# Kernel optimization log

Hardware: AMD Instinct MI355X
Metric: run time of the kernel (lower is better)

The kernel has to match this reference:

```python
import jax, jax.numpy as jnp
import numpy as np

NUM_GROUP = 512
GROUP_SIZE = 32


def setup_inputs() -> dict:
    key = jax.random.key(0)
    pts = jax.random.normal(key, (8, 8192, 6), dtype=jnp.float32)
    return {"pts": pts}


def _fps(xyz, num_group):
    """Farthest point sampling. xyz: (B, N, 3) -> indices (B, G)."""
    B, N, _ = xyz.shape

    def body(carry, _):
        dist, far = carry  # dist: (B, N) running min sq-dist to chosen set; far: (B,)
        centroid = jnp.take_along_axis(xyz, far[:, None, None], axis=1)  # (B, 1, 3)
        d = jnp.sum((xyz - centroid) ** 2, axis=-1)  # (B, N)
        dist = jnp.minimum(dist, d)
        new_far = jnp.argmax(dist, axis=-1)  # (B,)
        return (dist, new_far), far

    init = (jnp.full((B, N), 1e10, dtype=xyz.dtype), jnp.zeros((B,), dtype=jnp.int32))
    _, idxs = jax.lax.scan(body, init, None, length=num_group)  # (G, B)
    return idxs.T  # (B, G)


def _knn(k, xyz, center):
    """k nearest neighbors of each center among xyz. Returns idx (B, G, k)."""
    # squared distances (B, G, N)
    d2 = (jnp.sum(center ** 2, -1)[:, :, None]
          + jnp.sum(xyz ** 2, -1)[:, None, :]
          - 2.0 * jnp.einsum('bgc,bnc->bgn', center, xyz))
    _, idx = jax.lax.top_k(-d2, k)
    return idx


def reference(pts):
    xyz = pts[:, :, :3].astype(jnp.float32)
    fps_idx = _fps(xyz, NUM_GROUP)  # (B, G)
    center = jnp.take_along_axis(xyz, fps_idx[:, :, None], axis=1)  # (B, G, 3)
    idx = _knn(GROUP_SIZE, xyz, center)  # (B, G, K)
    # gather neighborhoods per batch: pts (B, N, C), idx (B, G, K) -> (B, G, K, C)
    neighborhood = jax.vmap(lambda p, i: p[i])(pts, idx)
    # center only the xyz channels
    nb_xyz = neighborhood[..., :3] - center[:, :, None, :]
    neighborhood = jnp.concatenate([nb_xyz, neighborhood[..., 3:]], axis=-1)
    return (neighborhood, center)
```

## Files before the change

### kernel.cpp

```cpp
#include <hip/hip_runtime.h>
#include <stdint.h>

#define BATCH 8
#define NPTS 8192
#define NGRP 512
#define KNN 32
#define NCH 6

#define FPS_T 512
#define FPS_PPT (NPTS / FPS_T)
#define PAIRS (FPS_PPT / 2)
#define FPS_NW (FPS_T / 64)

typedef float f2 __attribute__((ext_vector_type(2)));

__device__ __forceinline__ f2 pk_add(f2 a, f2 b) {
    f2 d;
    asm("v_pk_add_f32 %0, %1, %2" : "=v"(d) : "v"(a), "v"(b));
    return d;
}
__device__ __forceinline__ f2 pk_mul(f2 a, f2 b) {
    f2 d;
    asm("v_pk_mul_f32 %0, %1, %2" : "=v"(d) : "v"(a), "v"(b));
    return d;
}

template <int CTRL>
__device__ __forceinline__ float dpp_fmax(float v) {
    int s = __builtin_amdgcn_update_dpp(__float_as_int(v), __float_as_int(v),
                                        CTRL, 0xF, 0xF, false);
    return fmaxf(v, __int_as_float(s));
}

__global__ __launch_bounds__(FPS_T) void fps_kernel(const float* __restrict__ pts,
                                                    float* __restrict__ out_ctr) {
    __shared__ float xs[NPTS], ys[NPTS], zs[NPTS];
    __shared__ float ctr_lds[NGRP * 3];
    __shared__ float wslot[FPS_NW];
    __shared__ unsigned int islot[2];

    const int b   = blockIdx.x;
    const int tid = threadIdx.x;
    const float* base = pts + (size_t)b * NPTS * NCH;

    f2 x2[PAIRS], y2[PAIRS], z2[PAIRS], dist2[PAIRS];
#pragma unroll
    for (int i = 0; i < PAIRS; ++i) {
        int p0 = tid + (2 * i) * FPS_T;
        int p1 = tid + (2 * i + 1) * FPS_T;
        float xa = base[p0 * NCH + 0], ya = base[p0 * NCH + 1], za = base[p0 * NCH + 2];
        float xb = base[p1 * NCH + 0], yb = base[p1 * NCH + 1], zb = base[p1 * NCH + 2];
        x2[i] = (f2){xa, xb};
        y2[i] = (f2){ya, yb};
        z2[i] = (f2){za, zb};
        dist2[i] = (f2){1e10f, 1e10f};
        xs[p0] = xa; ys[p0] = ya; zs[p0] = za;
        xs[p1] = xb; ys[p1] = yb; zs[p1] = zb;
    }
    __syncthreads();

    int far = 0;
    const int wid  = tid >> 6;
    const int lane = tid & 63;

    for (int g = 0; g < NGRP; ++g) {
        float cx = xs[far], cy = ys[far], cz = zs[far];
        if (tid == 0) {
            ctr_lds[g * 3 + 0] = cx;
            ctr_lds[g * 3 + 1] = cy;
            ctr_lds[g * 3 + 2] = cz;
            islot[g & 1] = 0xFFFFFFFFu;
        }
        f2 ncx = (f2){-cx, -cx};
        f2 ncy = (f2){-cy, -cy};
        f2 ncz = (f2){-cz, -cz};

        float bestv = -1.0f;
#pragma unroll
        for (int i = 0; i < PAIRS; ++i) {
            f2 dx = pk_add(x2[i], ncx);
            f2 dy = pk_add(y2[i], ncy);
            f2 dz = pk_add(z2[i], ncz);
            f2 sx = pk_mul(dx, dx);
            f2 sy = pk_mul(dy, dy);
            f2 t  = pk_add(sx, sy);
            f2 sz = pk_mul(dz, dz);
            f2 d  = pk_add(t, sz);
            float nd0 = fminf(dist2[i].x, d.x);
            float nd1 = fminf(dist2[i].y, d.y);
            dist2[i].x = nd0;
            dist2[i].y = nd1;
            bestv = fmaxf(fmaxf(nd0, nd1), bestv);
        }

        float m = bestv;
        m = dpp_fmax<0x111>(m);
        m = dpp_fmax<0x112>(m);
        m = dpp_fmax<0x114>(m);
        m = dpp_fmax<0x118>(m);
        m = dpp_fmax<0x142>(m);
        m = dpp_fmax<0x143>(m);
        if (lane == 63) wslot[wid] = m;
        __syncthreads();

        float M = wslot[0];
#pragma unroll
        for (int w = 1; w < FPS_NW; ++w) M = fmaxf(M, wslot[w]);

        if (bestv == M) {
            int bj = 0;
#pragma unroll
            for (int i = PAIRS - 1; i >= 0; --i) {
                if (dist2[i].y == M) bj = 2 * i + 1;
                if (dist2[i].x == M) bj = 2 * i;
            }
            atomicMin(&islot[g & 1], (unsigned)(tid + bj * FPS_T));
        }
        __syncthreads();
        far = (int)islot[g & 1];
    }

    float* ctr = out_ctr + (size_t)b * NGRP * 3;
    for (int i = tid; i < NGRP * 3; i += FPS_T) ctr[i] = ctr_lds[i];
}

__device__ __forceinline__ unsigned long long knn_key(const float* __restrict__ base,
                                                      int p, float cx, float cy,
                                                      float cz, float cc) {
    float x = base[p * NCH + 0];
    float y = base[p * NCH + 1];
    float z = base[p * NCH + 2];
    float xx = __fadd_rn(__fadd_rn(__fmul_rn(x, x), __fmul_rn(y, y)), __fmul_rn(z, z));
    float dt = fmaf(cz, z, fmaf(cy, y, __fmul_rn(cx, x)));
    float d2 = __fsub_rn(__fadd_rn(cc, xx), __fmul_rn(2.0f, dt));
    unsigned int bits = __float_as_uint(d2);
    unsigned int ord = bits ^ ((unsigned)((int)bits >> 31) | 0x80000000u);
    return ((unsigned long long)ord << 13) | (unsigned)p;
}

__global__ __launch_bounds__(64) void knn_kernel(const float* __restrict__ pts,
                                                 const float* __restrict__ ctr,
                                                 float* __restrict__ out_nb) {
    const int bg   = blockIdx.x;
    const int b    = bg >> 9;
    const int lane = threadIdx.x & 63;
    const float* base = pts + (size_t)b * NPTS * NCH;

    const float cx = ctr[bg * 3 + 0];
    const float cy = ctr[bg * 3 + 1];
    const float cz = ctr[bg * 3 + 2];
    const float cc = __fadd_rn(__fadd_rn(__fmul_rn(cx, cx), __fmul_rn(cy, cy)),
                               __fmul_rn(cz, cz));

    unsigned long long R = knn_key(base, lane, cx, cy, cz, cc);
#pragma unroll
    for (int k = 2; k <= 64; k <<= 1) {
#pragma unroll
        for (int j = k >> 1; j > 0; j >>= 1) {
            unsigned long long o = __shfl_xor(R, j, 64);
            bool takeMin = (((lane & k) == 0) == ((lane & j) == 0));
            unsigned long long mn = (o < R) ? o : R;
            unsigned long long mx = (o < R) ? R : o;
            R = takeMin ? mn : mx;
        }
    }
    unsigned long long R31 = __shfl(R, 31, 64);

    for (int c = 1; c < NPTS / 64; ++c) {
        unsigned long long key = knn_key(base, c * 64 + lane, cx, cy, cz, cc);
        unsigned long long qual = __ballot(key < R31);
        while (qual) {
            int src = __ffsll(qual) - 1;
            qual &= qual - 1;
            unsigned long long bk = __shfl(key, src, 64);
            int rank = __popcll(__ballot(R < bk));
            unsigned long long Rp = __shfl_up(R, 1, 64);
            R = (lane == rank) ? bk : ((lane > rank) ? Rp : R);
            R31 = __shfl(R, 31, 64);
        }
    }

    if (lane < KNN) {
        int idx = (int)(R & 8191ULL);
        const float* s = base + (size_t)idx * NCH;
        float* d = out_nb + ((size_t)bg * KNN + lane) * NCH;
        d[0] = s[0] - cx;
        d[1] = s[1] - cy;
        d[2] = s[2] - cz;
        d[3] = s[3];
        d[4] = s[4];
        d[5] = s[5];
    }
}

extern "C" void kernel_launch(void* const* d_in, const int* in_sizes, int n_in,
                              void* d_out, int out_size, void* d_ws, size_t ws_size,
                              hipStream_t stream) {
    const float* pts = (const float*)d_in[0];
    float* out = (float*)d_out;
    float* out_nb  = out;
    float* out_ctr = out + (size_t)BATCH * NGRP * KNN * NCH;

    hipLaunchKernelGGL(fps_kernel, dim3(BATCH), dim3(FPS_T), 0, stream, pts, out_ctr);
    hipLaunchKernelGGL(knn_kernel, dim3(BATCH * NGRP), dim3(64), 0, stream,
                       pts, out_ctr, out_nb);
}
```

Baseline: 572.7 us.

## Fuse FPS and KNN into persistent kernel overlapping via global flags

Merges the farthest-point-sampling and KNN kernels into one persistent launch. Eight blocks run FPS and publish each chosen index to a workspace flag array, while the remaining blocks' waves spin on those flags and start KNN for each center as soon as it is available, overlapping the serial FPS with KNN work. FPS block size drops to 256 threads, and the argmax now reduces a packed 64-bit value/index key with DPP, removing the second barrier and the LDS atomicMin. This depends on all blocks being co-resident to avoid deadlock, and it adds a memset plus polling overhead.

```diff
diff --git a/kernel.cpp b/kernel.cpp
--- a/kernel.cpp
+++ b/kernel.cpp
@@ -7,10 +7,13 @@
 #define KNN 32
 #define NCH 6
 
-#define FPS_T 512
+#define FPS_T 256
 #define FPS_PPT (NPTS / FPS_T)
 #define PAIRS (FPS_PPT / 2)
 #define FPS_NW (FPS_T / 64)
+
+#define NBLK 248
+#define KNN_WAVES ((NBLK - BATCH) * FPS_NW)
 
 typedef float f2 __attribute__((ext_vector_type(2)));
 
@@ -26,102 +29,14 @@
 }
 
 template <int CTRL>
-__device__ __forceinline__ float dpp_fmax(float v) {
-    int s = __builtin_amdgcn_update_dpp(__float_as_int(v), __float_as_int(v),
-                                        CTRL, 0xF, 0xF, false);
-    return fmaxf(v, __int_as_float(s));
-}
-
-__global__ __launch_bounds__(FPS_T) void fps_kernel(const float* __restrict__ pts,
-                                                    float* __restrict__ out_ctr) {
-    __shared__ float xs[NPTS], ys[NPTS], zs[NPTS];
-    __shared__ float ctr_lds[NGRP * 3];
-    __shared__ float wslot[FPS_NW];
-    __shared__ unsigned int islot[2];
-
-    const int b   = blockIdx.x;
-    const int tid = threadIdx.x;
-    const float* base = pts + (size_t)b * NPTS * NCH;
-
-    f2 x2[PAIRS], y2[PAIRS], z2[PAIRS], dist2[PAIRS];
-#pragma unroll
-    for (int i = 0; i < PAIRS; ++i) {
-        int p0 = tid + (2 * i) * FPS_T;
-        int p1 = tid + (2 * i + 1) * FPS_T;
-        float xa = base[p0 * NCH + 0], ya = base[p0 * NCH + 1], za = base[p0 * NCH + 2];
-        float xb = base[p1 * NCH + 0], yb = base[p1 * NCH + 1], zb = base[p1 * NCH + 2];
-        x2[i] = (f2){xa, xb};
-        y2[i] = (f2){ya, yb};
-        z2[i] = (f2){za, zb};
-        dist2[i] = (f2){1e10f, 1e10f};
-        xs[p0] = xa; ys[p0] = ya; zs[p0] = za;
-        xs[p1] = xb; ys[p1] = yb; zs[p1] = zb;
-    }
-    __syncthreads();
-
-    int far = 0;
-    const int wid  = tid >> 6;
-    const int lane = tid & 63;
-
-    for (int g = 0; g < NGRP; ++g) {
-        float cx = xs[far], cy = ys[far], cz = zs[far];
-        if (tid == 0) {
-            ctr_lds[g * 3 + 0] = cx;
-            ctr_lds[g * 3 + 1] = cy;
-            ctr_lds[g * 3 + 2] = cz;
-            islot[g & 1] = 0xFFFFFFFFu;
-        }
-        f2 ncx = (f2){-cx, -cx};
-        f2 ncy = (f2){-cy, -cy};
-        f2 ncz = (f2){-cz, -cz};
-
-        float bestv = -1.0f;
-#pragma unroll
-        for (int i = 0; i < PAIRS; ++i) {
-            f2 dx = pk_add(x2[i], ncx);
-            f2 dy = pk_add(y2[i], ncy);
-            f2 dz = pk_add(z2[i], ncz);
-            f2 sx = pk_mul(dx, dx);
-            f2 sy = pk_mul(dy, dy);
-            f2 t  = pk_add(sx, sy);
-            f2 sz = pk_mul(dz, dz);
-            f2 d  = pk_add(t, sz);
-            float nd0 = fminf(dist2[i].x, d.x);
-            float nd1 = fminf(dist2[i].y, d.y);
-            dist2[i].x = nd0;
-            dist2[i].y = nd1;
-            bestv = fmaxf(fmaxf(nd0, nd1), bestv);
-        }
-
-        float m = bestv;
-        m = dpp_fmax<0x111>(m);
-        m = dpp_fmax<0x112>(m);
-        m = dpp_fmax<0x114>(m);
-        m = dpp_fmax<0x118>(m);
-        m = dpp_fmax<0x142>(m);
-        m = dpp_fmax<0x143>(m);
-        if (lane == 63) wslot[wid] = m;
-        __syncthreads();
-
-        float M = wslot[0];
-#pragma unroll
-        for (int w = 1; w < FPS_NW; ++w) M = fmaxf(M, wslot[w]);
-
-        if (bestv == M) {
-            int bj = 0;
-#pragma unroll
-            for (int i = PAIRS - 1; i >= 0; --i) {
-                if (dist2[i].y == M) bj = 2 * i + 1;
-                if (dist2[i].x == M) bj = 2 * i;
-            }
-            atomicMin(&islot[g & 1], (unsigned)(tid + bj * FPS_T));
-        }
-        __syncthreads();
-        far = (int)islot[g & 1];
-    }
-
-    float* ctr = out_ctr + (size_t)b * NGRP * 3;
-    for (int i = tid; i < NGRP * 3; i += FPS_T) ctr[i] = ctr_lds[i];
+__device__ __forceinline__ unsigned long long dpp_max64(unsigned long long k) {
+    int lo = (int)(unsigned)k;
+    int hi = (int)(unsigned)(k >> 32);
+    int plo = __builtin_amdgcn_update_dpp(lo, lo, CTRL, 0xF, 0xF, false);
+    int phi = __builtin_amdgcn_update_dpp(hi, hi, CTRL, 0xF, 0xF, false);
+    unsigned long long o =
+        ((unsigned long long)(unsigned)phi << 32) | (unsigned)plo;
+    return (o > k) ? o : k;
 }
 
 __device__ __forceinline__ unsigned long long knn_key(const float* __restrict__ base,
@@ -138,58 +53,168 @@
     return ((unsigned long long)ord << 13) | (unsigned)p;
 }
 
-__global__ __launch_bounds__(64) void knn_kernel(const float* __restrict__ pts,
-                                                 const float* __restrict__ ctr,
-                                                 float* __restrict__ out_nb) {
-    const int bg   = blockIdx.x;
-    const int b    = bg >> 9;
-    const int lane = threadIdx.x & 63;
-    const float* base = pts + (size_t)b * NPTS * NCH;
-
-    const float cx = ctr[bg * 3 + 0];
-    const float cy = ctr[bg * 3 + 1];
-    const float cz = ctr[bg * 3 + 2];
-    const float cc = __fadd_rn(__fadd_rn(__fmul_rn(cx, cx), __fmul_rn(cy, cy)),
-                               __fmul_rn(cz, cz));
-
-    unsigned long long R = knn_key(base, lane, cx, cy, cz, cc);
-#pragma unroll
-    for (int k = 2; k <= 64; k <<= 1) {
-#pragma unroll
-        for (int j = k >> 1; j > 0; j >>= 1) {
-            unsigned long long o = __shfl_xor(R, j, 64);
-            bool takeMin = (((lane & k) == 0) == ((lane & j) == 0));
-            unsigned long long mn = (o < R) ? o : R;
-            unsigned long long mx = (o < R) ? R : o;
-            R = takeMin ? mn : mx;
+__global__ __launch_bounds__(FPS_T) void fused_kernel(const float* __restrict__ pts,
+                                                      float* __restrict__ out_ctr,
+                                                      float* __restrict__ out_nb,
+                                                      unsigned int* __restrict__ faridx,
+                                                      int fstride) {
+    __shared__ float xs[NPTS], ys[NPTS], zs[NPTS];
+    __shared__ float ctr_lds[NGRP * 3];
+    __shared__ unsigned long long slots[2][FPS_NW];
+
+    const int tid = threadIdx.x;
+
+    if (blockIdx.x < BATCH) {
+        const int b = blockIdx.x;
+        const float* base = pts + (size_t)b * NPTS * NCH;
+
+        f2 x2[PAIRS], y2[PAIRS], z2[PAIRS], dist2[PAIRS];
+#pragma unroll
+        for (int i = 0; i < PAIRS; ++i) {
+            int p0 = tid + (2 * i) * FPS_T;
+            int p1 = tid + (2 * i + 1) * FPS_T;
+            float xa = base[p0 * NCH + 0], ya = base[p0 * NCH + 1], za = base[p0 * NCH + 2];
+            float xb = base[p1 * NCH + 0], yb = base[p1 * NCH + 1], zb = base[p1 * NCH + 2];
+            x2[i] = (f2){xa, xb};
+            y2[i] = (f2){ya, yb};
+            z2[i] = (f2){za, zb};
+            dist2[i] = (f2){1e10f, 1e10f};
+            xs[p0] = xa; ys[p0] = ya; zs[p0] = za;
+            xs[p1] = xb; ys[p1] = yb; zs[p1] = zb;
         }
-    }
-    unsigned long long R31 = __shfl(R, 31, 64);
-
-    for (int c = 1; c < NPTS / 64; ++c) {
-        unsigned long long key = knn_key(base, c * 64 + lane, cx, cy, cz, cc);
-        unsigned long long qual = __ballot(key < R31);
-        while (qual) {
-            int src = __ffsll(qual) - 1;
-            qual &= qual - 1;
-            unsigned long long bk = __shfl(key, src, 64);
-            int rank = __popcll(__ballot(R < bk));
-            unsigned long long Rp = __shfl_up(R, 1, 64);
-            R = (lane == rank) ? bk : ((lane > rank) ? Rp : R);
-            R31 = __shfl(R, 31, 64);
+        __syncthreads();
+
+        int far = 0;
+        const int wid  = tid >> 6;
+        const int lane = tid & 63;
+
+        for (int g = 0; g < NGRP; ++g) {
+            float cx = xs[far], cy = ys[far], cz = zs[far];
+            if (tid == 0) {
+                ctr_lds[g * 3 + 0] = cx;
+                ctr_lds[g * 3 + 1] = cy;
+                ctr_lds[g * 3 + 2] = cz;
+                __hip_atomic_store(&faridx[(b * NGRP + g) * fstride], (unsigned)far,
+                                   __ATOMIC_RELAXED, __HIP_MEMORY_SCOPE_AGENT);
+            }
+            if (g == NGRP - 1) break;
+
+            f2 ncx = (f2){-cx, -cx};
+            f2 ncy = (f2){-cy, -cy};
+            f2 ncz = (f2){-cz, -cz};
+
+            float bestv = -1.0f;
+            int bestj = 0;
+#pragma unroll
+            for (int i = 0; i < PAIRS; ++i) {
+                f2 dx = pk_add(x2[i], ncx);
+                f2 dy = pk_add(y2[i], ncy);
+                f2 dz = pk_add(z2[i], ncz);
+                f2 sx = pk_mul(dx, dx);
+                f2 sy = pk_mul(dy, dy);
+                f2 t  = pk_add(sx, sy);
+                f2 sz = pk_mul(dz, dz);
+                f2 d  = pk_add(t, sz);
+                float nd0 = fminf(dist2[i].x, d.x);
+                float nd1 = fminf(dist2[i].y, d.y);
+                dist2[i].x = nd0;
+                dist2[i].y = nd1;
+                if (nd0 > bestv) { bestv = nd0; bestj = 2 * i; }
+                if (nd1 > bestv) { bestv = nd1; bestj = 2 * i + 1; }
+            }
+            int bestp = tid + bestj * FPS_T;
+            unsigned long long key =
+                ((unsigned long long)__float_as_uint(bestv) << 13) |
+                (unsigned)(8191 - bestp);
+
+            key = dpp_max64<0x111>(key);
+            key = dpp_max64<0x112>(key);
+            key = dpp_max64<0x114>(key);
+            key = dpp_max64<0x118>(key);
+            key = dpp_max64<0x142>(key);
+            key = dpp_max64<0x143>(key);
+            if (lane == 63) slots[g & 1][wid] = key;
+            __syncthreads();
+
+            unsigned long long best = slots[g & 1][0];
+#pragma unroll
+            for (int w = 1; w < FPS_NW; ++w) {
+                unsigned long long o = slots[g & 1][w];
+                best = (o > best) ? o : best;
+            }
+            far = 8191 - (int)(best & 8191ULL);
         }
-    }
-
-    if (lane < KNN) {
-        int idx = (int)(R & 8191ULL);
-        const float* s = base + (size_t)idx * NCH;
-        float* d = out_nb + ((size_t)bg * KNN + lane) * NCH;
-        d[0] = s[0] - cx;
-        d[1] = s[1] - cy;
-        d[2] = s[2] - cz;
-        d[3] = s[3];
-        d[4] = s[4];
-        d[5] = s[5];
+
+        __syncthreads();
+        float* ctr = out_ctr + (size_t)b * NGRP * 3;
+        for (int i = tid; i < NGRP * 3; i += FPS_T) ctr[i] = ctr_lds[i];
+
+    } else {
+        const int wid  = tid >> 6;
+        const int lane = tid & 63;
+        const int W = (blockIdx.x - BATCH) * FPS_NW + wid;
+
+        for (int e = W; e < BATCH * NGRP; e += KNN_WAVES) {
+            const int g  = e >> 3;
+            const int b  = e & 7;
+            const int bg = b * NGRP + g;
+            const float* base = pts + (size_t)b * NPTS * NCH;
+
+            unsigned fidx;
+            if (lane == 0) {
+                while ((fidx = __hip_atomic_load(&faridx[bg * fstride],
+                                                 __ATOMIC_RELAXED,
+                                                 __HIP_MEMORY_SCOPE_AGENT)) == 0xFFFFFFFFu)
+                    __builtin_amdgcn_s_sleep(8);
+            }
+            fidx = (unsigned)__shfl((int)fidx, 0, 64);
+
+            const float cx = base[fidx * NCH + 0];
+            const float cy = base[fidx * NCH + 1];
+            const float cz = base[fidx * NCH + 2];
+            const float cc = __fadd_rn(__fadd_rn(__fmul_rn(cx, cx), __fmul_rn(cy, cy)),
+                                       __fmul_rn(cz, cz));
+
+            unsigned long long R = knn_key(base, lane, cx, cy, cz, cc);
+#pragma unroll
+            for (int k = 2; k <= 64; k <<= 1) {
+#pragma unroll
+                for (int j = k >> 1; j > 0; j >>= 1) {
+                    unsigned long long o = __shfl_xor(R, j, 64);
+                    bool takeMin = (((lane & k) == 0) == ((lane & j) == 0));
+                    unsigned long long mn = (o < R) ? o : R;
+                    unsigned long long mx = (o < R) ? R : o;
+                    R = takeMin ? mn : mx;
+                }
+            }
+            unsigned long long R31 = __shfl(R, 31, 64);
+
+            for (int c = 1; c < NPTS / 64; ++c) {
+                unsigned long long key = knn_key(base, c * 64 + lane, cx, cy, cz, cc);
+                unsigned long long qual = __ballot(key < R31);
+                while (qual) {
+                    int src = __ffsll(qual) - 1;
+                    qual &= qual - 1;
+                    unsigned long long bk = __shfl(key, src, 64);
+                    int rank = __popcll(__ballot(R < bk));
+                    unsigned long long Rp = __shfl_up(R, 1, 64);
+                    R = (lane == rank) ? bk : ((lane > rank) ? Rp : R);
+                    R31 = __shfl(R, 31, 64);
+                }
+            }
+
+            if (lane < KNN) {
+                int idx = (int)(R & 8191ULL);
+                const float* s = base + (size_t)idx * NCH;
+                float* d = out_nb + ((size_t)bg * KNN + lane) * NCH;
+                d[0] = s[0] - cx;
+                d[1] = s[1] - cy;
+                d[2] = s[2] - cz;
+                d[3] = s[3];
+                d[4] = s[4];
+                d[5] = s[5];
+            }
+        }
     }
 }
 
@@ -201,7 +226,11 @@
     float* out_nb  = out;
     float* out_ctr = out + (size_t)BATCH * NGRP * KNN * NCH;
 
-    hipLaunchKernelGGL(fps_kernel, dim3(BATCH), dim3(FPS_T), 0, stream, pts, out_ctr);
-    hipLaunchKernelGGL(knn_kernel, dim3(BATCH * NGRP), dim3(64), 0, stream,
-                       pts, out_ctr, out_nb);
-}
+    const size_t nctr = (size_t)BATCH * NGRP;
+    int fstride = (ws_size >= nctr * 16 * sizeof(unsigned)) ? 16 : 1;
+    unsigned int* faridx = (unsigned int*)d_ws;
+
+    hipMemsetAsync(d_ws, 0xFF, nctr * (size_t)fstride * sizeof(unsigned), stream);
+    hipLaunchKernelGGL(fused_kernel, dim3(NBLK), dim3(FPS_T), 0, stream,
+                       pts, out_ctr, out_nb, faridx, fstride);
+}
```

Result: faster. 513.2 us (-10.4%).
